# Kernel tuning notes

Hardware: AMD Instinct MI355X
Metric: run time of the kernel (lower is better)

Reference implementation:

```python
import jax, jax.numpy as jnp
import numpy as np

NUM_CLASSES = 3
EXCEPT_THRESH = 0.05
NMS_THRESH = 0.5
NMS_TOPK = 500
BATCH = 16
ANCHORS_PER_LOC = 3


def _make_scale(key, grid, stride):
    """Build realistic YOLO-style output / anchor / offset / stride tensors for one scale."""
    A = ANCHORS_PER_LOC
    N = grid * grid * A
    out = jax.random.normal(key, (BATCH, N, 5 + NUM_CLASSES), dtype=jnp.float32)
    ys, xs = jnp.meshgrid(jnp.arange(grid, dtype=jnp.float32),
                          jnp.arange(grid, dtype=jnp.float32), indexing='ij')
    off = jnp.stack([xs, ys], axis=-1).reshape(grid * grid, 1, 2)         # (G*G,1,2)
    off = jnp.broadcast_to(off, (grid * grid, A, 2)).reshape(1, N, 2)
    base = jnp.array([[16., 16.], [32., 24.], [24., 48.]], jnp.float32) * (stride / 8.0)
    anc = jnp.broadcast_to(base.reshape(1, 1, A, 2), (1, grid * grid, A, 2)).reshape(1, N, 2)
    st = jnp.full((1, 1, 2), stride, dtype=jnp.float32)
    return out, anc, off, st


def setup_inputs() -> dict:
    key = jax.random.key(0)
    k1, k2, k3 = jax.random.split(key, 3)
    o1, a1, f1, s1 = _make_scale(k1, 96, 8.0)
    o2, a2, f2, s2 = _make_scale(k2, 48, 16.0)
    o3, a3, f3, s3 = _make_scale(k3, 24, 32.0)
    return {
        'output1': o1, 'output2': o2, 'output3': o3,
        'anchor1': a1, 'anchor2': a2, 'anchor3': a3,
        'offset1': f1, 'offset2': f2, 'offset3': f3,
        'stride1': s1, 'stride2': s2, 'stride3': s3,
    }


def _decode(out, anchor, offset, stride):
    """YOLOv3 multiperclass decode -> (B, N*C, 6) rows of [id, score, x1, y1, x2, y2]."""
    xy, wh = out[..., 0:2], out[..., 2:4]
    obj, cls = out[..., 4:5], out[..., 5:]
    # from_sigmoid=False: apply sigmoid to centers / objectness / class logits
    xy = jax.nn.sigmoid(xy)
    obj = jax.nn.sigmoid(obj)
    cls = jax.nn.sigmoid(cls)
    center = (xy + offset) * stride              # (B,N,2)
    half = 0.5 * jnp.exp(wh) * anchor            # (B,N,2)
    bbox = jnp.concatenate([center - half, center + half], axis=-1)  # (B,N,4)
    scores = obj * cls                           # (B,N,C)
    B, N, C = scores.shape
    ids = jnp.broadcast_to(jnp.arange(C, dtype=jnp.float32), (B, N, C))
    mask = scores > EXCEPT_THRESH
    ids = jnp.where(mask, ids, -1.0)
    scr = jnp.where(mask, scores, -1.0)
    bb = jnp.broadcast_to(bbox[:, :, None, :], (B, N, C, 4))
    res = jnp.concatenate([ids[..., None], scr[..., None], bb], axis=-1)
    return res.reshape(B, N * C, 6)


def _iou_matrix(boxes):
    """boxes (K,4) corner format -> (K,K) IoU."""
    x1, y1, x2, y2 = boxes[:, 0], boxes[:, 1], boxes[:, 2], boxes[:, 3]
    area = jnp.maximum(x2 - x1, 0.0) * jnp.maximum(y2 - y1, 0.0)
    iw = jnp.maximum(jnp.minimum(x2[:, None], x2[None]) - jnp.maximum(x1[:, None], x1[None]), 0.0)
    ih = jnp.maximum(jnp.minimum(y2[:, None], y2[None]) - jnp.maximum(y1[:, None], y1[None]), 0.0)
    inter = iw * ih
    return inter / (area[:, None] + area[None] - inter + 1e-12)


def _greedy_keep(iou, valid):
    """Greedy NMS over score-sorted candidates. iou (K,K), valid (K,) -> keep (K,) bool."""
    K = iou.shape[0]
    ar = jnp.arange(K)
    def body(i, keep):
        suppressed = jnp.any(keep & (ar < i) & (iou[i] > NMS_THRESH))
        return keep.at[i].set(valid[i] & ~suppressed)
    return jax.lax.fori_loop(0, K, body, valid)


def _per_class_nms(ids, scores, bboxes):
    """ids/scores (B,M,1), bboxes (B,M,4). Suppressed candidates get id=-1, score=-1.
    uid=-1 (background / below-threshold) entries pass through untouched, matching the
    original which skips NMS for uid<0."""
    B, M = ids.shape[:2]
    idf, scf = ids[..., 0], scores[..., 0]
    scatter = jax.vmap(lambda kf, o, k: kf.at[o].set(k))
    for c in range(NUM_CLASSES):
        cmask = idf == float(c)
        s = jnp.where(cmask, scf, -jnp.inf)
        order = jnp.argsort(-s, axis=1)[:, :NMS_TOPK]            # (B,K)
        sb = jnp.take_along_axis(s, order, axis=1)               # (B,K)
        bb = jnp.take_along_axis(bboxes, order[..., None], axis=1)  # (B,K,4)
        valid = jnp.isfinite(sb)
        iou = jax.vmap(_iou_matrix)(bb)                          # (B,K,K)
        keep = jax.vmap(_greedy_keep)(iou, valid)                # (B,K)
        keep_full = scatter(jnp.zeros((B, M), bool), order, keep)
        sup = cmask & ~keep_full                                 # suppressed or beyond topk
        idf = jnp.where(sup, -1.0, idf)
        scf = jnp.where(sup, -1.0, scf)
    return idf[..., None], scf[..., None], bboxes


def reference(output1, output2, output3, anchor1, anchor2, anchor3,
              offset1, offset2, offset3, stride1, stride2, stride3):
    results = jnp.concatenate([
        _decode(output1, anchor1, offset1, stride1),
        _decode(output2, anchor2, offset2, stride2),
        _decode(output3, anchor3, offset3, stride3),
    ], axis=1)                                   # (B, M, 6)
    ids = results[:, :, 0:1]
    scores = results[:, :, 1:2]
    bboxes = results[:, :, 2:]
    return _per_class_nms(ids, scores, bboxes)
```

## Files before the change

### kernel.cpp

```cpp
#include <hip/hip_runtime.h>

#define N1 27648
#define N2 6912
#define N3 1728
#define NTOT 36288
#define BATCH_ 16
#define C_ 3
#define GRP (BATCH_ * C_)
#define MROWS (NTOT * C_)
#define TOPK 500
#define NBINS 2304
#define CCAP 2048
#define BASEBITS 0x3D400000u
#define TPRE 0.5f
#define LISTCAP 4096
#define CNT_STRIDE 32

#define OFF_LIST   8192ull
#define SZ_LIST    ((size_t)GRP * LISTCAP * 8)
#define OFF_KEYS   (OFF_LIST + SZ_LIST)
#define SZ_KEYS    ((size_t)GRP * 512 * 8)
#define OFF_BOXES  (OFF_KEYS + SZ_KEYS)
#define SZ_BOXES   ((size_t)GRP * 512 * 16)
#define OFF_MASKS  (OFF_BOXES + SZ_BOXES)
#define SZ_MASKS   ((size_t)GRP * 4096 * 8)
#define OFF_KCNT   (OFF_MASKS + SZ_MASKS)
#define SZ_KCNT    4096ull
#define WS_NEED    (OFF_KCNT + SZ_KCNT)

typedef float f4_t __attribute__((ext_vector_type(4)));

__device__ __forceinline__ float sigm(float x) { return 1.0f / (1.0f + expf(-x)); }

__device__ __forceinline__ float score_of(int b, int n, int c,
    const float* __restrict__ o1, const float* __restrict__ o2, const float* __restrict__ o3)
{
    const float* o; int ln, Ns;
    if (n < N1)           { o = o1; ln = n;             Ns = N1; }
    else if (n < N1 + N2) { o = o2; ln = n - N1;        Ns = N2; }
    else                  { o = o3; ln = n - (N1 + N2); Ns = N3; }
    const float* r = o + ((size_t)b * Ns + ln) * 8;
    return sigm(r[4]) * sigm(r[5 + c]);
}

__device__ __forceinline__ unsigned wave_push(bool pred, unsigned* cntp)
{
    unsigned long long mb = __ballot(pred);
    unsigned pos = 0xFFFFFFFFu;
    if (pred) {
        int lane = threadIdx.x & 63;
        int leader = __ffsll((long long)mb) - 1;
        unsigned total = (unsigned)__popcll(mb);
        unsigned base = 0;
        if (lane == leader) base = atomicAdd(cntp, total);
        base = __shfl(base, leader);
        pos = base + (unsigned)__popcll(mb & ((1ull << lane) - 1ull));
    }
    return pos;
}

__global__ __launch_bounds__(64) void zerocnt_kernel(unsigned* __restrict__ cnts)
{
    if (threadIdx.x < GRP) cnts[threadIdx.x * CNT_STRIDE] = 0u;
}

__global__ __launch_bounds__(256) void decode_filter_kernel(
    const float* __restrict__ o1, const float* __restrict__ o2, const float* __restrict__ o3,
    const float* __restrict__ a1, const float* __restrict__ a2, const float* __restrict__ a3,
    const float* __restrict__ f1, const float* __restrict__ f2, const float* __restrict__ f3,
    const float* __restrict__ s1, const float* __restrict__ s2, const float* __restrict__ s3,
    float* __restrict__ out,
    unsigned* __restrict__ cnts, unsigned long long* __restrict__ list, int listcap)
{
    __shared__ unsigned lcnt[C_];
    __shared__ unsigned lbase[C_];
    __shared__ unsigned long long stage[C_][256];

    const int tid = threadIdx.x;
    const int n = blockIdx.x * 256 + tid;
    const int b = blockIdx.y;
    const bool active = (n < NTOT);

    if (tid < C_) lcnt[tid] = 0u;
    __syncthreads();

    if (active) {
        const float *o, *anc, *off, *st; int ln, Ns;
        if (n < N1)           { o = o1; anc = a1; off = f1; st = s1; ln = n;             Ns = N1; }
        else if (n < N1 + N2) { o = o2; anc = a2; off = f2; st = s2; ln = n - N1;        Ns = N2; }
        else                  { o = o3; anc = a3; off = f3; st = s3; ln = n - (N1 + N2); Ns = N3; }
        const float* r = o + ((size_t)b * Ns + ln) * 8;
        float4 v0 = *(const float4*)r;
        float4 v1 = *(const float4*)(r + 4);

        float sx = sigm(v0.x);
        float sy = sigm(v0.y);
        float cx = (sx + off[2 * ln + 0]) * st[0];
        float cy = (sy + off[2 * ln + 1]) * st[1];
        float hx = 0.5f * expf(v0.z) * anc[2 * ln + 0];
        float hy = 0.5f * expf(v0.w) * anc[2 * ln + 1];
        f4_t bb = { cx - hx, cy - hy, cx + hx, cy + hy };

        size_t base = (size_t)b * MROWS + (size_t)n * C_;
        float* ids = out;
        float* scs = out + (size_t)BATCH_ * MROWS;
        float* bbs = out + 2ull * BATCH_ * MROWS;

        __builtin_nontemporal_store(-1.0f, &ids[base + 0]);
        __builtin_nontemporal_store(-1.0f, &ids[base + 1]);
        __builtin_nontemporal_store(-1.0f, &ids[base + 2]);
        __builtin_nontemporal_store(-1.0f, &scs[base + 0]);
        __builtin_nontemporal_store(-1.0f, &scs[base + 1]);
        __builtin_nontemporal_store(-1.0f, &scs[base + 2]);

        f4_t* bp = (f4_t*)(bbs + base * 4);
        __builtin_nontemporal_store(bb, bp + 0);
        __builtin_nontemporal_store(bb, bp + 1);
        __builtin_nontemporal_store(bb, bp + 2);

        if (listcap > 0) {
            float sobj = sigm(v1.x);
            float s[3] = { sobj * sigm(v1.y), sobj * sigm(v1.z), sobj * sigm(v1.w) };
            #pragma unroll
            for (int c = 0; c < C_; ++c) {
                if (s[c] > TPRE) {
                    unsigned p = atomicAdd(&lcnt[c], 1u);
                    stage[c][p] =
                        ((unsigned long long)__float_as_uint(s[c]) << 32) | (unsigned)(~n);
                }
            }
        }
    }

    if (listcap > 0) {
        __syncthreads();
        if (tid < C_)
            lbase[tid] = atomicAdd(&cnts[(b * C_ + tid) * CNT_STRIDE], lcnt[tid]);
        __syncthreads();
        #pragma unroll
        for (int c = 0; c < C_; ++c) {
            unsigned m = lcnt[c];
            if ((unsigned)tid < m) {
                unsigned pos = lbase[c] + (unsigned)tid;
                if (pos < (unsigned)listcap)
                    list[(size_t)(b * C_ + c) * listcap + pos] = stage[c][tid];
            }
        }
    }
}

__global__ __launch_bounds__(512) void topk_kernel(
    const float* __restrict__ o1, const float* __restrict__ o2, const float* __restrict__ o3,
    const float* __restrict__ out,
    const unsigned* __restrict__ cnts, const unsigned long long* __restrict__ list,
    unsigned long long* __restrict__ gkeys, float4* __restrict__ gboxes,
    unsigned* __restrict__ kcnt)
{
    const int g = blockIdx.x;
    const int b = g / C_;
    const int c = g - b * C_;
    const int tid = threadIdx.x;

    __shared__ unsigned long long keys[CCAP];
    __shared__ unsigned int hist[NBINS];
    __shared__ unsigned int sh_tb, sh_cnt;

    unsigned cnt_g = cnts[g * CNT_STRIDE];
    const bool pathL = (cnt_g >= TOPK && cnt_g <= (unsigned)LISTCAP);
    const unsigned long long* L = list + (size_t)g * LISTCAP;

    for (int i = tid; i < NBINS; i += 512) hist[i] = 0u;
    if (tid == 0) sh_cnt = 0u;
    __syncthreads();

    if (pathL) {
        #pragma unroll 4
        for (unsigned i = tid; i < cnt_g; i += 512) {
            unsigned bin = ((unsigned)(L[i] >> 32) - BASEBITS) >> 14;
            if (bin > NBINS - 1u) bin = NBINS - 1u;
            atomicAdd(&hist[bin], 1u);
        }
    } else {
        for (int n = tid; n < NTOT; n += 512) {
            float s = score_of(b, n, c, o1, o2, o3);
            if (s > 0.05f) {
                unsigned bin = (__float_as_uint(s) - BASEBITS) >> 14;
                if (bin > NBINS - 1u) bin = NBINS - 1u;
                atomicAdd(&hist[bin], 1u);
            }
        }
    }
    __syncthreads();

    if (tid < 64) {
        const int CHUNK = NBINS / 64;
        int base_i = tid * CHUNK;
        unsigned own = 0;
        #pragma unroll
        for (int k = 0; k < CHUNK; ++k) own += hist[base_i + k];
        unsigned sfx = own;
        #pragma unroll
        for (int off = 1; off < 64; off <<= 1) {
            unsigned v = __shfl_down(sfx, off, 64);
            sfx += (tid + off < 64) ? v : 0u;
        }
        unsigned sfxn = sfx - own;
        if (tid == 0 && sfx < TOPK) sh_tb = 0u;
        if (sfx >= TOPK && sfxn < TOPK) {
            unsigned cum = sfxn, tb = (unsigned)base_i;
            for (int k = CHUNK - 1; k >= 0; --k) {
                cum += hist[base_i + k];
                if (cum >= TOPK) { tb = (unsigned)(base_i + k); break; }
            }
            sh_tb = tb;
        }
    }
    __syncthreads();

    const unsigned tb = sh_tb;
    if (pathL) {
        unsigned nIter = (cnt_g + 511u) & ~511u;
        #pragma unroll 4
        for (unsigned i = tid; i < nIter; i += 512) {
            bool pred = false; unsigned long long key = 0ull;
            if (i < cnt_g) {
                key = L[i];
                unsigned bin = ((unsigned)(key >> 32) - BASEBITS) >> 14;
                if (bin > NBINS - 1u) bin = NBINS - 1u;
                pred = (bin >= tb);
            }
            unsigned p = wave_push(pred, &sh_cnt);
            if (pred && p < CCAP) keys[p] = key;
        }
    } else {
        const int nIter = (NTOT + 511) & ~511;
        for (int n = tid; n < nIter; n += 512) {
            bool pred = false; unsigned long long key = 0ull;
            if (n < NTOT) {
                float s = score_of(b, n, c, o1, o2, o3);
                if (s > 0.05f) {
                    unsigned bits = __float_as_uint(s);
                    unsigned bin = (bits - BASEBITS) >> 14;
                    if (bin > NBINS - 1u) bin = NBINS - 1u;
                    if (bin >= tb) {
                        pred = true;
                        key = ((unsigned long long)bits << 32) | (unsigned)(~n);
                    }
                }
            }
            unsigned p = wave_push(pred, &sh_cnt);
            if (pred && p < CCAP) keys[p] = key;
        }
    }
    __syncthreads();

    const unsigned cnt2 = min(sh_cnt, (unsigned)CCAP);
    unsigned S2 = 2;
    while (S2 < cnt2) S2 <<= 1;
    for (unsigned i = tid; i < S2; i += 512)
        if (i >= cnt2) keys[i] = 0ull;
    __syncthreads();

    for (unsigned k = 2; k <= S2; k <<= 1) {
        for (unsigned j = k >> 1; j > 0; j >>= 1) {
            for (unsigned i = tid; i < S2; i += 512) {
                unsigned ixj = i ^ j;
                if (ixj > i) {
                    unsigned long long x = keys[i], y = keys[ixj];
                    bool desc = ((i & k) == 0);
                    if (desc ? (x < y) : (x > y)) { keys[i] = y; keys[ixj] = x; }
                }
            }
            __syncthreads();
        }
    }

    const int K = (int)min(cnt2, (unsigned)TOPK);

    if (tid == 0) kcnt[g] = (unsigned)K;
    if (tid < K) {
        unsigned long long key = keys[tid];
        gkeys[(size_t)g * 512 + tid] = key;
        unsigned idx = ~(unsigned)(key & 0xFFFFFFFFull);
        const float* bbs = out + 2ull * BATCH_ * MROWS;
        gboxes[(size_t)g * 512 + tid] =
            *(const float4*)(bbs + ((size_t)b * MROWS + (size_t)idx * C_) * 4);
    }
}

__global__ __launch_bounds__(256) void masks_kernel(
    const float4* __restrict__ gboxes, const unsigned* __restrict__ kcnt,
    unsigned long long* __restrict__ gmasks)
{
    const int g = blockIdx.x;
    const int w = blockIdx.y;
    const int K = (int)kcnt[g];

    __shared__ float bx[TOPK * 4];
    __shared__ float ar[TOPK];

    const float4* B = gboxes + (size_t)g * 512;
    for (int j = threadIdx.x; j < K; j += 256) {
        float4 v = B[j];
        bx[j*4+0] = v.x; bx[j*4+1] = v.y; bx[j*4+2] = v.z; bx[j*4+3] = v.w;
        ar[j] = fmaxf(v.z - v.x, 0.0f) * fmaxf(v.w - v.y, 0.0f);
    }
    __syncthreads();

    unsigned long long* M = gmasks + (size_t)g * 4096 + (size_t)w * 512;
    const int j0 = w * 64;
    const int jhi = (K < j0 + 64) ? K : j0 + 64;

    for (int i = threadIdx.x; i < K; i += 256) {
        unsigned long long word = 0ull;
        if (i + 1 < jhi) {
            float xi1 = bx[i*4+0], yi1 = bx[i*4+1], xi2 = bx[i*4+2], yi2 = bx[i*4+3];
            float ai = ar[i];
            for (int j = j0; j < jhi; ++j) {
                float xj1 = bx[j*4+0], yj1 = bx[j*4+1], xj2 = bx[j*4+2], yj2 = bx[j*4+3];
                float aj = ar[j];
                float iw = fmaxf(fminf(xi2, xj2) - fmaxf(xi1, xj1), 0.0f);
                float ih = fmaxf(fminf(yi2, yj2) - fmaxf(yi1, yj1), 0.0f);
                float inter = iw * ih;
                float iou = inter / (ai + aj - inter + 1e-12f);
                if (iou > 0.5f && j > i) word |= 1ull << (j - j0);
            }
        }
        M[i] = word;
    }
}

__global__ __launch_bounds__(512) void greedy_kernel(
    const unsigned long long* __restrict__ gmasks,
    const unsigned long long* __restrict__ gkeys,
    const unsigned* __restrict__ kcnt, float* __restrict__ out)
{
    const int g = blockIdx.x;
    const int b = g / C_;
    const int c = g - b * C_;
    const int tid = threadIdx.x;
    const int K = (int)kcnt[g];

    __shared__ unsigned long long mlds[512 * 9];
    __shared__ unsigned long long keep_s[8];

    const unsigned long long* GM = gmasks + (size_t)g * 4096;
    for (int t = tid; t < 8 * 512; t += 512) {
        int w = t >> 9, i = t & 511;
        mlds[i * 9 + w] = (i < K) ? GM[w * 512 + i] : 0ull;
    }
    __syncthreads();

    if (tid < 64) {
        const int lane8 = tid & 7;
        unsigned long long removed = 0ull, keep = 0ull;
        const int Kpad = (K + 7) & ~7;

        unsigned long long m0 = mlds[0*9+lane8], m1 = mlds[1*9+lane8],
                           m2 = mlds[2*9+lane8], m3 = mlds[3*9+lane8],
                           m4 = mlds[4*9+lane8], m5 = mlds[5*9+lane8],
                           m6 = mlds[6*9+lane8], m7 = mlds[7*9+lane8];

        for (int i0 = 0; i0 < Kpad; i0 += 8) {
            int nb = (i0 + 8 < 512) ? (i0 + 8) : 0;
            unsigned long long n0 = mlds[(nb+0)*9+lane8], n1 = mlds[(nb+1)*9+lane8],
                               n2 = mlds[(nb+2)*9+lane8], n3 = mlds[(nb+3)*9+lane8],
                               n4 = mlds[(nb+4)*9+lane8], n5 = mlds[(nb+5)*9+lane8],
                               n6 = mlds[(nb+6)*9+lane8], n7 = mlds[(nb+7)*9+lane8];

            #define GSTEP(t, mt) { \
                int i = i0 + t; \
                int w = i >> 6, bp = i & 63; \
                bool mine = (tid == w) && ((removed >> bp) & 1ull); \
                unsigned long long alive = __any(mine) ? 0ull : ~0ull; \
                keep |= ((tid == w) ? (1ull << bp) : 0ull) & alive; \
                removed |= mt & alive; \
            }
            GSTEP(0, m0) GSTEP(1, m1) GSTEP(2, m2) GSTEP(3, m3)
            GSTEP(4, m4) GSTEP(5, m5) GSTEP(6, m6) GSTEP(7, m7)
            #undef GSTEP

            m0=n0; m1=n1; m2=n2; m3=n3; m4=n4; m5=n5; m6=n6; m7=n7;
        }
        if (tid < 8) keep_s[tid] = keep;
    }
    __syncthreads();

    const unsigned long long* GK = gkeys + (size_t)g * 512;
    for (int i = tid; i < K; i += 512) {
        if ((keep_s[i >> 6] >> (i & 63)) & 1ull) {
            unsigned long long key = GK[i];
            unsigned idx = ~(unsigned)(key & 0xFFFFFFFFull);
            float sc = __uint_as_float((unsigned)(key >> 32));
            size_t row = (size_t)b * MROWS + (size_t)idx * C_ + c;
            out[row] = (float)c;
            out[(size_t)BATCH_ * MROWS + row] = sc;
        }
    }
}

__global__ __launch_bounds__(512) void select_nms_mono(
    const float* __restrict__ o1, const float* __restrict__ o2, const float* __restrict__ o3,
    float* __restrict__ out,
    const unsigned* __restrict__ cnts, const unsigned long long* __restrict__ list, int listcap)
{
    const int g = blockIdx.x;
    const int b = g / C_;
    const int c = g - b * C_;
    const int tid = threadIdx.x;

    __shared__ unsigned long long smem[7048];
    __shared__ unsigned int sh_tb, sh_cnt;
    __shared__ unsigned long long keepw[8];

    unsigned long long* keys = smem;
    unsigned int* hist = (unsigned int*)(smem + CCAP);
    float* boxes = (float*)(smem + CCAP);
    unsigned long long* masks = smem + 3048;

    unsigned cnt_g = 0;
    bool pathL = false;
    if (listcap >= TOPK) {
        cnt_g = cnts[g * CNT_STRIDE];
        pathL = (cnt_g >= TOPK && cnt_g <= (unsigned)listcap);
    }
    const unsigned long long* L = list + (size_t)g * (size_t)(listcap > 0 ? listcap : 1);

    for (int i = tid; i < NBINS; i += 512) hist[i] = 0u;
    if (tid == 0) sh_cnt = 0u;
    __syncthreads();

    if (pathL) {
        for (unsigned i = tid; i < cnt_g; i += 512) {
            unsigned bin = ((unsigned)(L[i] >> 32) - BASEBITS) >> 14;
            if (bin > NBINS - 1u) bin = NBINS - 1u;
            atomicAdd(&hist[bin], 1u);
        }
    } else {
        for (int n = tid; n < NTOT; n += 512) {
            float s = score_of(b, n, c, o1, o2, o3);
            if (s > 0.05f) {
                unsigned bin = (__float_as_uint(s) - BASEBITS) >> 14;
                if (bin > NBINS - 1u) bin = NBINS - 1u;
                atomicAdd(&hist[bin], 1u);
            }
        }
    }
    __syncthreads();

    if (tid < 64) {
        const int CHUNK = NBINS / 64;
        int base_i = tid * CHUNK;
        unsigned own = 0;
        #pragma unroll
        for (int k = 0; k < CHUNK; ++k) own += hist[base_i + k];
        unsigned sfx = own;
        #pragma unroll
        for (int off = 1; off < 64; off <<= 1) {
            unsigned v = __shfl_down(sfx, off, 64);
            sfx += (tid + off < 64) ? v : 0u;
        }
        unsigned sfxn = sfx - own;
        if (tid == 0 && sfx < TOPK) sh_tb = 0u;
        if (sfx >= TOPK && sfxn < TOPK) {
            unsigned cum = sfxn, tb = (unsigned)base_i;
            for (int k = CHUNK - 1; k >= 0; --k) {
                cum += hist[base_i + k];
                if (cum >= TOPK) { tb = (unsigned)(base_i + k); break; }
            }
            sh_tb = tb;
        }
    }
    __syncthreads();

    const unsigned tb = sh_tb;
    if (pathL) {
        for (unsigned i = tid; i < cnt_g; i += 512) {
            unsigned long long key = L[i];
            unsigned bin = ((unsigned)(key >> 32) - BASEBITS) >> 14;
            if (bin > NBINS - 1u) bin = NBINS - 1u;
            if (bin >= tb) {
                unsigned p = atomicAdd(&sh_cnt, 1u);
                if (p < CCAP) keys[p] = key;
            }
        }
    } else {
        for (int n = tid; n < NTOT; n += 512) {
            float s = score_of(b, n, c, o1, o2, o3);
            if (s > 0.05f) {
                unsigned bits = __float_as_uint(s);
                unsigned bin = (bits - BASEBITS) >> 14;
                if (bin > NBINS - 1u) bin = NBINS - 1u;
                if (bin >= tb) {
                    unsigned p = atomicAdd(&sh_cnt, 1u);
                    if (p < CCAP)
                        keys[p] = ((unsigned long long)bits << 32) | (unsigned)(~n);
                }
            }
        }
    }
    __syncthreads();

    const unsigned cnt2 = min(sh_cnt, (unsigned)CCAP);
    unsigned S2 = 2;
    while (S2 < cnt2) S2 <<= 1;
    for (unsigned i = tid; i < S2; i += 512)
        if (i >= cnt2) keys[i] = 0ull;
    __syncthreads();

    for (unsigned k = 2; k <= S2; k <<= 1) {
        for (unsigned j = k >> 1; j > 0; j >>= 1) {
            for (unsigned i = tid; i < S2; i += 512) {
                unsigned ixj = i ^ j;
                if (ixj > i) {
                    unsigned long long x = keys[i], y = keys[ixj];
                    bool desc = ((i & k) == 0);
                    if (desc ? (x < y) : (x > y)) { keys[i] = y; keys[ixj] = x; }
                }
            }
            __syncthreads();
        }
    }

    const int K = (int)min(cnt2, (unsigned)TOPK);

    {
        const float* bbs = out + 2ull * BATCH_ * MROWS;
        if (tid < K) {
            unsigned idx = ~(unsigned)(keys[tid] & 0xFFFFFFFFull);
            float4 bb = *(const float4*)(bbs + ((size_t)b * MROWS + (size_t)idx * C_) * 4);
            ((float4*)boxes)[tid] = bb;
        }
    }
    __syncthreads();

    {
        const int nw = (K + 63) >> 6;
        for (int t = tid; t < K * nw; t += 512) {
            int w = t / K;
            int i = t - w * K;
            float xi1 = boxes[i*4+0], yi1 = boxes[i*4+1], xi2 = boxes[i*4+2], yi2 = boxes[i*4+3];
            float ai = fmaxf(xi2 - xi1, 0.0f) * fmaxf(yi2 - yi1, 0.0f);
            unsigned long long word = 0ull;
            int jlo = (i + 1 > w * 64) ? i + 1 : w * 64;
            int jhi = (K < (w + 1) * 64) ? K : (w + 1) * 64;
            for (int j = jlo; j < jhi; ++j) {
                float xj1 = boxes[j*4+0], yj1 = boxes[j*4+1], xj2 = boxes[j*4+2], yj2 = boxes[j*4+3];
                float aj = fmaxf(xj2 - xj1, 0.0f) * fmaxf(yj2 - yj1, 0.0f);
                float iw = fmaxf(fminf(xi2, xj2) - fmaxf(xi1, xj1), 0.0f);
                float ih = fmaxf(fminf(yi2, yj2) - fmaxf(yi1, yj1), 0.0f);
                float inter = iw * ih;
                float iou = inter / (ai + aj - inter + 1e-12f);
                if (iou > 0.5f) word |= 1ull << (j & 63);
            }
            masks[i * 8 + w] = word;
        }
    }
    __syncthreads();

    if (tid < 64) {
        unsigned long long removed = 0ull, keep = 0ull;
        for (int i = 0; i < K; ++i) {
            unsigned long long mw = (tid < 8) ? masks[i * 8 + tid] : 0ull;
            int w = i >> 6, bp = i & 63;
            bool mine = (tid == w) && ((removed >> bp) & 1ull);
            if (!__any(mine)) {
                if (tid == w) keep |= 1ull << bp;
                removed |= mw;
            }
        }
        if (tid < 8) keepw[tid] = keep;
    }
    __syncthreads();

    if (tid < K && ((keepw[tid >> 6] >> (tid & 63)) & 1ull)) {
        unsigned long long key = keys[tid];
        unsigned idx = ~(unsigned)(key & 0xFFFFFFFFull);
        float sc = __uint_as_float((unsigned)(key >> 32));
        size_t row = (size_t)b * MROWS + (size_t)idx * C_ + c;
        out[row] = (float)c;
        out[(size_t)BATCH_ * MROWS + row] = sc;
    }
}

extern "C" void kernel_launch(void* const* d_in, const int* in_sizes, int n_in,
                              void* d_out, int out_size, void* d_ws, size_t ws_size,
                              hipStream_t stream)
{
    const float* o1 = (const float*)d_in[0];
    const float* o2 = (const float*)d_in[1];
    const float* o3 = (const float*)d_in[2];
    const float* a1 = (const float*)d_in[3];
    const float* a2 = (const float*)d_in[4];
    const float* a3 = (const float*)d_in[5];
    const float* f1 = (const float*)d_in[6];
    const float* f2 = (const float*)d_in[7];
    const float* f3 = (const float*)d_in[8];
    const float* s1 = (const float*)d_in[9];
    const float* s2 = (const float*)d_in[10];
    const float* s3 = (const float*)d_in[11];
    float* out = (float*)d_out;

    unsigned* cnts = (unsigned*)d_ws;
    const bool haveCnts = (ws_size >= (size_t)GRP * CNT_STRIDE * 4);

    if (haveCnts)
        zerocnt_kernel<<<dim3(1), dim3(64), 0, stream>>>(cnts);

    if (ws_size >= WS_NEED) {
        unsigned long long* list   = (unsigned long long*)((char*)d_ws + OFF_LIST);
        unsigned long long* gkeys  = (unsigned long long*)((char*)d_ws + OFF_KEYS);
        float4*             gboxes = (float4*)((char*)d_ws + OFF_BOXES);
        unsigned long long* gmasks = (unsigned long long*)((char*)d_ws + OFF_MASKS);
        unsigned*           kcnt   = (unsigned*)((char*)d_ws + OFF_KCNT);

        decode_filter_kernel<<<dim3((NTOT + 255) / 256, BATCH_), dim3(256), 0, stream>>>(
            o1, o2, o3, a1, a2, a3, f1, f2, f3, s1, s2, s3, out, cnts, list, LISTCAP);
        topk_kernel<<<dim3(GRP), dim3(512), 0, stream>>>(
            o1, o2, o3, out, cnts, list, gkeys, gboxes, kcnt);
        masks_kernel<<<dim3(GRP, 8), dim3(256), 0, stream>>>(gboxes, kcnt, gmasks);
        greedy_kernel<<<dim3(GRP), dim3(512), 0, stream>>>(gmasks, gkeys, kcnt, out);
    } else {
        unsigned long long* list = (unsigned long long*)((char*)d_ws + OFF_LIST);
        int listcap = 0;
        if (haveCnts && ws_size >= OFF_LIST + (size_t)GRP * TOPK * 8) {
            size_t cap = (ws_size - OFF_LIST) / (8ull * GRP);
            listcap = (int)(cap > LISTCAP ? LISTCAP : cap);
        }
        decode_filter_kernel<<<dim3((NTOT + 255) / 256, BATCH_), dim3(256), 0, stream>>>(
            o1, o2, o3, a1, a2, a3, f1, f2, f3, s1, s2, s3, out, cnts, list, listcap);
        select_nms_mono<<<dim3(GRP), dim3(512), 0, stream>>>(
            o1, o2, o3, out, cnts, list, listcap);
    }
}
```

Before: 100.3 us.

## Replace global atomic candidate list with per-block segments and drop zeroing kernel

```diff
diff --git a/kernel.cpp b/kernel.cpp
--- a/kernel.cpp
+++ b/kernel.cpp
@@ -13,12 +13,14 @@
 #define CCAP 2048
 #define BASEBITS 0x3D400000u
 #define TPRE 0.5f
-#define LISTCAP 4096
-#define CNT_STRIDE 32
-
-#define OFF_LIST   8192ull
-#define SZ_LIST    ((size_t)GRP * LISTCAP * 8)
-#define OFF_KEYS   (OFF_LIST + SZ_LIST)
+#define BLKX 142
+#define SEGCAP 96
+
+#define OFF_CNT    0ull
+#define SZ_CNT     32768ull
+#define OFF_SEG    (OFF_CNT + SZ_CNT)
+#define SZ_SEG     ((size_t)GRP * BLKX * SEGCAP * 8)
+#define OFF_KEYS   (OFF_SEG + SZ_SEG)
 #define SZ_KEYS    ((size_t)GRP * 512 * 8)
 #define OFF_BOXES  (OFF_KEYS + SZ_KEYS)
 #define SZ_BOXES   ((size_t)GRP * 512 * 16)
@@ -27,8 +29,6 @@
 #define OFF_KCNT   (OFF_MASKS + SZ_MASKS)
 #define SZ_KCNT    4096ull
 #define WS_NEED    (OFF_KCNT + SZ_KCNT)
-
-typedef float f4_t __attribute__((ext_vector_type(4)));
 
 __device__ __forceinline__ float sigm(float x) { return 1.0f / (1.0f + expf(-x)); }
 
@@ -59,139 +59,10 @@
     return pos;
 }
 
-__global__ __launch_bounds__(64) void zerocnt_kernel(unsigned* __restrict__ cnts)
-{
-    if (threadIdx.x < GRP) cnts[threadIdx.x * CNT_STRIDE] = 0u;
-}
-
-__global__ __launch_bounds__(256) void decode_filter_kernel(
-    const float* __restrict__ o1, const float* __restrict__ o2, const float* __restrict__ o3,
-    const float* __restrict__ a1, const float* __restrict__ a2, const float* __restrict__ a3,
-    const float* __restrict__ f1, const float* __restrict__ f2, const float* __restrict__ f3,
-    const float* __restrict__ s1, const float* __restrict__ s2, const float* __restrict__ s3,
-    float* __restrict__ out,
-    unsigned* __restrict__ cnts, unsigned long long* __restrict__ list, int listcap)
-{
-    __shared__ unsigned lcnt[C_];
-    __shared__ unsigned lbase[C_];
-    __shared__ unsigned long long stage[C_][256];
-
+__device__ __forceinline__ void scan_tb(const unsigned* hist,
+                                        unsigned* sh_tb, unsigned* sh_tot)
+{
     const int tid = threadIdx.x;
-    const int n = blockIdx.x * 256 + tid;
-    const int b = blockIdx.y;
-    const bool active = (n < NTOT);
-
-    if (tid < C_) lcnt[tid] = 0u;
-    __syncthreads();
-
-    if (active) {
-        const float *o, *anc, *off, *st; int ln, Ns;
-        if (n < N1)           { o = o1; anc = a1; off = f1; st = s1; ln = n;             Ns = N1; }
-        else if (n < N1 + N2) { o = o2; anc = a2; off = f2; st = s2; ln = n - N1;        Ns = N2; }
-        else                  { o = o3; anc = a3; off = f3; st = s3; ln = n - (N1 + N2); Ns = N3; }
-        const float* r = o + ((size_t)b * Ns + ln) * 8;
-        float4 v0 = *(const float4*)r;
-        float4 v1 = *(const float4*)(r + 4);
-
-        float sx = sigm(v0.x);
-        float sy = sigm(v0.y);
-        float cx = (sx + off[2 * ln + 0]) * st[0];
-        float cy = (sy + off[2 * ln + 1]) * st[1];
-        float hx = 0.5f * expf(v0.z) * anc[2 * ln + 0];
-        float hy = 0.5f * expf(v0.w) * anc[2 * ln + 1];
-        f4_t bb = { cx - hx, cy - hy, cx + hx, cy + hy };
-
-        size_t base = (size_t)b * MROWS + (size_t)n * C_;
-        float* ids = out;
-        float* scs = out + (size_t)BATCH_ * MROWS;
-        float* bbs = out + 2ull * BATCH_ * MROWS;
-
-        __builtin_nontemporal_store(-1.0f, &ids[base + 0]);
-        __builtin_nontemporal_store(-1.0f, &ids[base + 1]);
-        __builtin_nontemporal_store(-1.0f, &ids[base + 2]);
-        __builtin_nontemporal_store(-1.0f, &scs[base + 0]);
-        __builtin_nontemporal_store(-1.0f, &scs[base + 1]);
-        __builtin_nontemporal_store(-1.0f, &scs[base + 2]);
-
-        f4_t* bp = (f4_t*)(bbs + base * 4);
-        __builtin_nontemporal_store(bb, bp + 0);
-        __builtin_nontemporal_store(bb, bp + 1);
-        __builtin_nontemporal_store(bb, bp + 2);
-
-        if (listcap > 0) {
-            float sobj = sigm(v1.x);
-            float s[3] = { sobj * sigm(v1.y), sobj * sigm(v1.z), sobj * sigm(v1.w) };
-            #pragma unroll
-            for (int c = 0; c < C_; ++c) {
-                if (s[c] > TPRE) {
-                    unsigned p = atomicAdd(&lcnt[c], 1u);
-                    stage[c][p] =
-                        ((unsigned long long)__float_as_uint(s[c]) << 32) | (unsigned)(~n);
-                }
-            }
-        }
-    }
-
-    if (listcap > 0) {
-        __syncthreads();
-        if (tid < C_)
-            lbase[tid] = atomicAdd(&cnts[(b * C_ + tid) * CNT_STRIDE], lcnt[tid]);
-        __syncthreads();
-        #pragma unroll
-        for (int c = 0; c < C_; ++c) {
-            unsigned m = lcnt[c];
-            if ((unsigned)tid < m) {
-                unsigned pos = lbase[c] + (unsigned)tid;
-                if (pos < (unsigned)listcap)
-                    list[(size_t)(b * C_ + c) * listcap + pos] = stage[c][tid];
-            }
-        }
-    }
-}
-
-__global__ __launch_bounds__(512) void topk_kernel(
-    const float* __restrict__ o1, const float* __restrict__ o2, const float* __restrict__ o3,
-    const float* __restrict__ out,
-    const unsigned* __restrict__ cnts, const unsigned long long* __restrict__ list,
-    unsigned long long* __restrict__ gkeys, float4* __restrict__ gboxes,
-    unsigned* __restrict__ kcnt)
-{
-    const int g = blockIdx.x;
-    const int b = g / C_;
-    const int c = g - b * C_;
-    const int tid = threadIdx.x;
-
-    __shared__ unsigned long long keys[CCAP];
-    __shared__ unsigned int hist[NBINS];
-    __shared__ unsigned int sh_tb, sh_cnt;
-
-    unsigned cnt_g = cnts[g * CNT_STRIDE];
-    const bool pathL = (cnt_g >= TOPK && cnt_g <= (unsigned)LISTCAP);
-    const unsigned long long* L = list + (size_t)g * LISTCAP;
-
-    for (int i = tid; i < NBINS; i += 512) hist[i] = 0u;
-    if (tid == 0) sh_cnt = 0u;
-    __syncthreads();
-
-    if (pathL) {
-        #pragma unroll 4
-        for (unsigned i = tid; i < cnt_g; i += 512) {
-            unsigned bin = ((unsigned)(L[i] >> 32) - BASEBITS) >> 14;
-            if (bin > NBINS - 1u) bin = NBINS - 1u;
-            atomicAdd(&hist[bin], 1u);
-        }
-    } else {
-        for (int n = tid; n < NTOT; n += 512) {
-            float s = score_of(b, n, c, o1, o2, o3);
-            if (s > 0.05f) {
-                unsigned bin = (__float_as_uint(s) - BASEBITS) >> 14;
-                if (bin > NBINS - 1u) bin = NBINS - 1u;
-                atomicAdd(&hist[bin], 1u);
-            }
-        }
-    }
-    __syncthreads();
-
     if (tid < 64) {
         const int CHUNK = NBINS / 64;
         int base_i = tid * CHUNK;
@@ -205,29 +76,170 @@
             sfx += (tid + off < 64) ? v : 0u;
         }
         unsigned sfxn = sfx - own;
-        if (tid == 0 && sfx < TOPK) sh_tb = 0u;
+        if (tid == 0) { *sh_tot = sfx; if (sfx < TOPK) *sh_tb = 0u; }
         if (sfx >= TOPK && sfxn < TOPK) {
             unsigned cum = sfxn, tb = (unsigned)base_i;
             for (int k = CHUNK - 1; k >= 0; --k) {
                 cum += hist[base_i + k];
                 if (cum >= TOPK) { tb = (unsigned)(base_i + k); break; }
             }
-            sh_tb = tb;
-        }
-    }
-    __syncthreads();
+            *sh_tb = tb;
+        }
+    }
+}
+
+__global__ __launch_bounds__(256) void decode_filter_kernel(
+    const float* __restrict__ o1, const float* __restrict__ o2, const float* __restrict__ o3,
+    const float* __restrict__ a1, const float* __restrict__ a2, const float* __restrict__ a3,
+    const float* __restrict__ f1, const float* __restrict__ f2, const float* __restrict__ f3,
+    const float* __restrict__ s1, const float* __restrict__ s2, const float* __restrict__ s3,
+    float* __restrict__ out,
+    unsigned* __restrict__ cntArr, unsigned long long* __restrict__ seg)
+{
+    __shared__ unsigned lcnt[C_];
+    __shared__ unsigned long long stage[C_][256];
+
+    const int tid = threadIdx.x;
+    const int x = blockIdx.x;
+    const int n = x * 256 + tid;
+    const int b = blockIdx.y;
+
+    if (tid < C_) lcnt[tid] = 0u;
+    __syncthreads();
+
+    if (n < NTOT) {
+        const float *o, *anc, *off, *st; int ln, Ns;
+        if (n < N1)           { o = o1; anc = a1; off = f1; st = s1; ln = n;             Ns = N1; }
+        else if (n < N1 + N2) { o = o2; anc = a2; off = f2; st = s2; ln = n - N1;        Ns = N2; }
+        else                  { o = o3; anc = a3; off = f3; st = s3; ln = n - (N1 + N2); Ns = N3; }
+        const float* r = o + ((size_t)b * Ns + ln) * 8;
+        float4 v0 = *(const float4*)r;
+        float4 v1 = *(const float4*)(r + 4);
+
+        float sx = sigm(v0.x);
+        float sy = sigm(v0.y);
+        float cx = (sx + off[2 * ln + 0]) * st[0];
+        float cy = (sy + off[2 * ln + 1]) * st[1];
+        float hx = 0.5f * expf(v0.z) * anc[2 * ln + 0];
+        float hy = 0.5f * expf(v0.w) * anc[2 * ln + 1];
+        float4 bb = make_float4(cx - hx, cy - hy, cx + hx, cy + hy);
+
+        size_t base = (size_t)b * MROWS + (size_t)n * C_;
+        float* ids = out;
+        float* scs = out + (size_t)BATCH_ * MROWS;
+        float* bbs = out + 2ull * BATCH_ * MROWS;
+
+        __builtin_nontemporal_store(-1.0f, &ids[base + 0]);
+        __builtin_nontemporal_store(-1.0f, &ids[base + 1]);
+        __builtin_nontemporal_store(-1.0f, &ids[base + 2]);
+        __builtin_nontemporal_store(-1.0f, &scs[base + 0]);
+        __builtin_nontemporal_store(-1.0f, &scs[base + 1]);
+        __builtin_nontemporal_store(-1.0f, &scs[base + 2]);
+        float4* bp = (float4*)(bbs + base * 4);
+        bp[0] = bb; bp[1] = bb; bp[2] = bb;
+
+        if (cntArr != nullptr) {
+            float sobj = sigm(v1.x);
+            float s[3] = { sobj * sigm(v1.y), sobj * sigm(v1.z), sobj * sigm(v1.w) };
+            #pragma unroll
+            for (int c = 0; c < C_; ++c) {
+                if (s[c] > TPRE) {
+                    unsigned p = atomicAdd(&lcnt[c], 1u);
+                    stage[c][p] =
+                        ((unsigned long long)__float_as_uint(s[c]) << 32) | (unsigned)(~n);
+                }
+            }
+        }
+    }
+
+    if (cntArr != nullptr) {
+        __syncthreads();
+        if (tid < C_)
+            cntArr[(b * C_ + tid) * BLKX + x] = lcnt[tid];
+        #pragma unroll
+        for (int c = 0; c < C_; ++c) {
+            unsigned m = lcnt[c];
+            if (m > SEGCAP) m = SEGCAP;
+            if ((unsigned)tid < m)
+                seg[((size_t)(b * C_ + c) * BLKX + x) * SEGCAP + tid] = stage[c][tid];
+        }
+    }
+}
+
+__global__ __launch_bounds__(512) void topk_kernel(
+    const float* __restrict__ o1, const float* __restrict__ o2, const float* __restrict__ o3,
+    const float* __restrict__ out,
+    const unsigned* __restrict__ cntArr, const unsigned long long* __restrict__ seg,
+    unsigned long long* __restrict__ gkeys, float4* __restrict__ gboxes,
+    unsigned* __restrict__ kcnt)
+{
+    const int g = blockIdx.x;
+    const int b = g / C_;
+    const int c = g - b * C_;
+    const int tid = threadIdx.x;
+
+    __shared__ unsigned long long keys[CCAP];
+    __shared__ unsigned int hist[NBINS];
+    __shared__ unsigned int sh_tb, sh_tot, sh_cnt, sh_flag;
+
+    const unsigned* CNT = cntArr + g * BLKX;
+    const unsigned long long* SEG = seg + (size_t)g * BLKX * SEGCAP;
+
+    if (tid == 0) { sh_cnt = 0u; sh_flag = 0u; }
+    for (int i = tid; i < NBINS; i += 512) hist[i] = 0u;
+    __syncthreads();
+    {
+        unsigned ovf = 0;
+        for (int x = tid; x < BLKX; x += 512)
+            if (CNT[x] > SEGCAP) ovf = 1;
+        if (ovf) atomicOr(&sh_flag, 1u);
+    }
+    __syncthreads();
+    bool useRaw = (sh_flag != 0u);
+
+    if (!useRaw) {
+        for (int t = tid; t < BLKX * SEGCAP; t += 512) {
+            int x = t / SEGCAP, slot = t - x * SEGCAP;
+            if (slot < (int)CNT[x]) {
+                unsigned bin = ((unsigned)(SEG[t] >> 32) - BASEBITS) >> 14;
+                if (bin > NBINS - 1u) bin = NBINS - 1u;
+                atomicAdd(&hist[bin], 1u);
+            }
+        }
+        __syncthreads();
+        scan_tb(hist, &sh_tb, &sh_tot);
+        __syncthreads();
+        if (sh_tot < TOPK) useRaw = true;
+    }
+    if (useRaw) {
+        for (int i = tid; i < NBINS; i += 512) hist[i] = 0u;
+        __syncthreads();
+        for (int n = tid; n < NTOT; n += 512) {
+            float s = score_of(b, n, c, o1, o2, o3);
+            if (s > 0.05f) {
+                unsigned bin = (__float_as_uint(s) - BASEBITS) >> 14;
+                if (bin > NBINS - 1u) bin = NBINS - 1u;
+                atomicAdd(&hist[bin], 1u);
+            }
+        }
+        __syncthreads();
+        scan_tb(hist, &sh_tb, &sh_tot);
+        __syncthreads();
+    }
 
     const unsigned tb = sh_tb;
-    if (pathL) {
-        unsigned nIter = (cnt_g + 511u) & ~511u;
-        #pragma unroll 4
-        for (unsigned i = tid; i < nIter; i += 512) {
+    if (!useRaw) {
+        const int nIter = (BLKX * SEGCAP + 511) & ~511;
+        for (int t = tid; t < nIter; t += 512) {
             bool pred = false; unsigned long long key = 0ull;
-            if (i < cnt_g) {
-                key = L[i];
-                unsigned bin = ((unsigned)(key >> 32) - BASEBITS) >> 14;
-                if (bin > NBINS - 1u) bin = NBINS - 1u;
-                pred = (bin >= tb);
+            if (t < BLKX * SEGCAP) {
+                int x = t / SEGCAP, slot = t - x * SEGCAP;
+                if (slot < (int)CNT[x]) {
+                    key = SEG[t];
+                    unsigned bin = ((unsigned)(key >> 32) - BASEBITS) >> 14;
+                    if (bin > NBINS - 1u) bin = NBINS - 1u;
+                    pred = (bin >= tb);
+                }
             }
             unsigned p = wave_push(pred, &sh_cnt);
             if (pred && p < CCAP) keys[p] = key;
@@ -401,8 +413,7 @@
 
 __global__ __launch_bounds__(512) void select_nms_mono(
     const float* __restrict__ o1, const float* __restrict__ o2, const float* __restrict__ o3,
-    float* __restrict__ out,
-    const unsigned* __restrict__ cnts, const unsigned long long* __restrict__ list, int listcap)
+    float* __restrict__ out)
 {
     const int g = blockIdx.x;
     const int b = g / C_;
@@ -410,7 +421,7 @@
     const int tid = threadIdx.x;
 
     __shared__ unsigned long long smem[7048];
-    __shared__ unsigned int sh_tb, sh_cnt;
+    __shared__ unsigned int sh_tb, sh_tot, sh_cnt;
     __shared__ unsigned long long keepw[8];
 
     unsigned long long* keys = smem;
@@ -418,84 +429,33 @@
     float* boxes = (float*)(smem + CCAP);
     unsigned long long* masks = smem + 3048;
 
-    unsigned cnt_g = 0;
-    bool pathL = false;
-    if (listcap >= TOPK) {
-        cnt_g = cnts[g * CNT_STRIDE];
-        pathL = (cnt_g >= TOPK && cnt_g <= (unsigned)listcap);
-    }
-    const unsigned long long* L = list + (size_t)g * (size_t)(listcap > 0 ? listcap : 1);
-
     for (int i = tid; i < NBINS; i += 512) hist[i] = 0u;
     if (tid == 0) sh_cnt = 0u;
     __syncthreads();
 
-    if (pathL) {
-        for (unsigned i = tid; i < cnt_g; i += 512) {
-            unsigned bin = ((unsigned)(L[i] >> 32) - BASEBITS) >> 14;
+    for (int n = tid; n < NTOT; n += 512) {
+        float s = score_of(b, n, c, o1, o2, o3);
+        if (s > 0.05f) {
+            unsigned bin = (__float_as_uint(s) - BASEBITS) >> 14;
             if (bin > NBINS - 1u) bin = NBINS - 1u;
             atomicAdd(&hist[bin], 1u);
         }
-    } else {
-        for (int n = tid; n < NTOT; n += 512) {
-            float s = score_of(b, n, c, o1, o2, o3);
-            if (s > 0.05f) {
-                unsigned bin = (__float_as_uint(s) - BASEBITS) >> 14;
-                if (bin > NBINS - 1u) bin = NBINS - 1u;
-                atomicAdd(&hist[bin], 1u);
-            }
-        }
-    }
-    __syncthreads();
-
-    if (tid < 64) {
-        const int CHUNK = NBINS / 64;
-        int base_i = tid * CHUNK;
-        unsigned own = 0;
-        #pragma unroll
-        for (int k = 0; k < CHUNK; ++k) own += hist[base_i + k];
-        unsigned sfx = own;
-        #pragma unroll
-        for (int off = 1; off < 64; off <<= 1) {
-            unsigned v = __shfl_down(sfx, off, 64);
-            sfx += (tid + off < 64) ? v : 0u;
-        }
-        unsigned sfxn = sfx - own;
-        if (tid == 0 && sfx < TOPK) sh_tb = 0u;
-        if (sfx >= TOPK && sfxn < TOPK) {
-            unsigned cum = sfxn, tb = (unsigned)base_i;
-            for (int k = CHUNK - 1; k >= 0; --k) {
-                cum += hist[base_i + k];
-                if (cum >= TOPK) { tb = (unsigned)(base_i + k); break; }
-            }
-            sh_tb = tb;
-        }
-    }
+    }
+    __syncthreads();
+    scan_tb(hist, &sh_tb, &sh_tot);
     __syncthreads();
 
     const unsigned tb = sh_tb;
-    if (pathL) {
-        for (unsigned i = tid; i < cnt_g; i += 512) {
-            unsigned long long key = L[i];
-            unsigned bin = ((unsigned)(key >> 32) - BASEBITS) >> 14;
+    for (int n = tid; n < NTOT; n += 512) {
+        float s = score_of(b, n, c, o1, o2, o3);
+        if (s > 0.05f) {
+            unsigned bits = __float_as_uint(s);
+            unsigned bin = (bits - BASEBITS) >> 14;
             if (bin > NBINS - 1u) bin = NBINS - 1u;
             if (bin >= tb) {
                 unsigned p = atomicAdd(&sh_cnt, 1u);
-                if (p < CCAP) keys[p] = key;
-            }
-        }
-    } else {
-        for (int n = tid; n < NTOT; n += 512) {
-            float s = score_of(b, n, c, o1, o2, o3);
-            if (s > 0.05f) {
-                unsigned bits = __float_as_uint(s);
-                unsigned bin = (bits - BASEBITS) >> 14;
-                if (bin > NBINS - 1u) bin = NBINS - 1u;
-                if (bin >= tb) {
-                    unsigned p = atomicAdd(&sh_cnt, 1u);
-                    if (p < CCAP)
-                        keys[p] = ((unsigned long long)bits << 32) | (unsigned)(~n);
-                }
+                if (p < CCAP)
+                    keys[p] = ((unsigned long long)bits << 32) | (unsigned)(~n);
             }
         }
     }
@@ -601,35 +561,23 @@
     const float* s3 = (const float*)d_in[11];
     float* out = (float*)d_out;
 
-    unsigned* cnts = (unsigned*)d_ws;
-    const bool haveCnts = (ws_size >= (size_t)GRP * CNT_STRIDE * 4);
-
-    if (haveCnts)
-        zerocnt_kernel<<<dim3(1), dim3(64), 0, stream>>>(cnts);
-
     if (ws_size >= WS_NEED) {
-        unsigned long long* list   = (unsigned long long*)((char*)d_ws + OFF_LIST);
+        unsigned*           cntArr = (unsigned*)((char*)d_ws + OFF_CNT);
+        unsigned long long* seg    = (unsigned long long*)((char*)d_ws + OFF_SEG);
         unsigned long long* gkeys  = (unsigned long long*)((char*)d_ws + OFF_KEYS);
         float4*             gboxes = (float4*)((char*)d_ws + OFF_BOXES);
         unsigned long long* gmasks = (unsigned long long*)((char*)d_ws + OFF_MASKS);
         unsigned*           kcnt   = (unsigned*)((char*)d_ws + OFF_KCNT);
 
-        decode_filter_kernel<<<dim3((NTOT + 255) / 256, BATCH_), dim3(256), 0, stream>>>(
-            o1, o2, o3, a1, a2, a3, f1, f2, f3, s1, s2, s3, out, cnts, list, LISTCAP);
+        decode_filter_kernel<<<dim3(BLKX, BATCH_), dim3(256), 0, stream>>>(
+            o1, o2, o3, a1, a2, a3, f1, f2, f3, s1, s2, s3, out, cntArr, seg);
         topk_kernel<<<dim3(GRP), dim3(512), 0, stream>>>(
-            o1, o2, o3, out, cnts, list, gkeys, gboxes, kcnt);
+            o1, o2, o3, out, cntArr, seg, gkeys, gboxes, kcnt);
         masks_kernel<<<dim3(GRP, 8), dim3(256), 0, stream>>>(gboxes, kcnt, gmasks);
         greedy_kernel<<<dim3(GRP), dim3(512), 0, stream>>>(gmasks, gkeys, kcnt, out);
     } else {
-        unsigned long long* list = (unsigned long long*)((char*)d_ws + OFF_LIST);
-        int listcap = 0;
-        if (haveCnts && ws_size >= OFF_LIST + (size_t)GRP * TOPK * 8) {
-            size_t cap = (ws_size - OFF_LIST) / (8ull * GRP);
-            listcap = (int)(cap > LISTCAP ? LISTCAP : cap);
-        }
-        decode_filter_kernel<<<dim3((NTOT + 255) / 256, BATCH_), dim3(256), 0, stream>>>(
-            o1, o2, o3, a1, a2, a3, f1, f2, f3, s1, s2, s3, out, cnts, list, listcap);
-        select_nms_mono<<<dim3(GRP), dim3(512), 0, stream>>>(
-            o1, o2, o3, out, cnts, list, listcap);
-    }
-}
+        decode_filter_kernel<<<dim3(BLKX, BATCH_), dim3(256), 0, stream>>>(
+            o1, o2, o3, a1, a2, a3, f1, f2, f3, s1, s2, s3, out, nullptr, nullptr);
+        select_nms_mono<<<dim3(GRP), dim3(512), 0, stream>>>(o1, o2, o3, out);
+    }
+}
```

New measurement: 108.9 us. +8.6%, slower.
